# Optimization experiments

Hardware: AMD Instinct MI355X
Metric: run time of the kernel (lower is better)

## Reference

```python
import jax, jax.numpy as jnp
import numpy as np

EMBED_DIM = 1024
NUM_HEADS = 16
HEAD_DIM = EMBED_DIM // NUM_HEADS  # 64
B, H_P, W_P = 4, 48, 48
N = H_P * W_P  # 2304


def setup_inputs() -> dict:
    key = jax.random.key(0)
    ks = jax.random.split(key, 12)
    s = 1.0 / np.sqrt(EMBED_DIM)
    inp = {
        "query": jax.random.normal(ks[0], (B, N, EMBED_DIM), jnp.float32),
        "key": jax.random.normal(ks[1], (B, N, EMBED_DIM), jnp.float32),
        "value": jax.random.normal(ks[2], (B, N, EMBED_DIM), jnp.float32),
        "Wq": jax.random.normal(ks[3], (EMBED_DIM, EMBED_DIM), jnp.float32) * s,
        "bq": jnp.zeros((EMBED_DIM,), jnp.float32),
        "Wk": jax.random.normal(ks[4], (EMBED_DIM, EMBED_DIM), jnp.float32) * s,
        "bk": jnp.zeros((EMBED_DIM,), jnp.float32),
        "Wv": jax.random.normal(ks[5], (EMBED_DIM, EMBED_DIM), jnp.float32) * s,
        "bv": jnp.zeros((EMBED_DIM,), jnp.float32),
        "Wo": jax.random.normal(ks[6], (EMBED_DIM, EMBED_DIM), jnp.float32) * s,
        "bo": jnp.zeros((EMBED_DIM,), jnp.float32),
        "H_patch": H_P,
        "W_patch": W_P,
    }
    return inp


def _rope_2d_cos_sin(h_idx, w_idx, head_dim):
    # 2D RoPE: first half of head_dim encodes the y axis, second half the x axis.
    half = head_dim // 2          # dims per spatial axis (32)
    inv_freq = 1.0 / (10000.0 ** (jnp.arange(0, half, 2, dtype=jnp.float32) / half))  # [half//2]
    fh = h_idx.astype(jnp.float32)[:, None] * inv_freq[None, :]  # [N, half//2]
    fw = w_idx.astype(jnp.float32)[:, None] * inv_freq[None, :]
    emb_h = jnp.concatenate([fh, fh], axis=-1)  # [N, half]
    emb_w = jnp.concatenate([fw, fw], axis=-1)
    emb = jnp.concatenate([emb_h, emb_w], axis=-1)  # [N, head_dim]
    return jnp.cos(emb), jnp.sin(emb)


def _rotate_half_seg(x):
    # rotate_half within a per-axis segment
    h = x.shape[-1] // 2
    return jnp.concatenate([-x[..., h:], x[..., :h]], axis=-1)


def _apply_rotary_2d(x, cos, sin):
    # x: [B, H, N, head_dim]; cos/sin: [N, head_dim]
    half = x.shape[-1] // 2
    c = cos[None, None]
    s = sin[None, None]
    xh, xw = x[..., :half], x[..., half:]
    ch, cw = c[..., :half], c[..., half:]
    sh, sw = s[..., :half], s[..., half:]
    yh = xh * ch + _rotate_half_seg(xh) * sh
    yw = xw * cw + _rotate_half_seg(xw) * sw
    return jnp.concatenate([yh, yw], axis=-1)


def reference(query, key, value, Wq, bq, Wk, bk, Wv, bv, Wo, bo, H_patch, W_patch):
    Bsz, Nn, D = query.shape
    hd = D // NUM_HEADS

    def split_heads(x):
        return x.reshape(Bsz, Nn, NUM_HEADS, hd).transpose(0, 2, 1, 3)  # [B,H,N,hd]

    q = split_heads(query @ Wq.T + bq)
    k = split_heads(key @ Wk.T + bk)
    v = split_heads(value @ Wv.T + bv)

    ys = jnp.arange(H_patch)
    xs = jnp.arange(W_patch)
    yy, xx = jnp.meshgrid(ys, xs, indexing="ij")
    cos, sin = _rope_2d_cos_sin(yy.reshape(-1), xx.reshape(-1), hd)

    q = _apply_rotary_2d(q, cos, sin)
    k = _apply_rotary_2d(k, cos, sin)

    scale = hd ** (-0.5)
    attn = jnp.einsum("bhnd,bhmd->bhnm", q, k) * scale
    attn = jax.nn.softmax(attn, axis=-1)
    out = jnp.einsum("bhnm,bhmd->bhnd", attn, v)
    out = out.transpose(0, 2, 1, 3).reshape(Bsz, Nn, D)
    return out @ Wo.T + bo
```

## Files before the change

kernel.cpp:

```cpp
#include <hip/hip_runtime.h>
#include <cstdint>
#include <cstddef>


typedef __bf16 bf16x8 __attribute__((ext_vector_type(8)));
typedef __bf16 bf16x4 __attribute__((ext_vector_type(4)));
typedef _Float16 f16x4 __attribute__((ext_vector_type(4)));
typedef _Float16 f16x8 __attribute__((ext_vector_type(8)));
typedef float f32x4 __attribute__((ext_vector_type(4)));

constexpr int Bc = 4, Hc = 16, Nc = 2304, Ec = 1024, WPc = 48;
constexpr int BNc = Bc * Nc;

__device__ __forceinline__ f32x4 mfma16(bf16x8 a, bf16x8 b, f32x4 c) {
  return __builtin_amdgcn_mfma_f32_16x16x32_bf16(a, b, c, 0, 0, 0);
}
__device__ __forceinline__ f32x4 mfmah32(f16x8 a, f16x8 b, f32x4 c) {
  return __builtin_amdgcn_mfma_f32_16x16x32_f16(a, b, c, 0, 0, 0);
}

#if __has_builtin(__builtin_amdgcn_exp2f)
#define EXP2F(x) __builtin_amdgcn_exp2f(x)
#else
#define EXP2F(x) exp2f(x)
#endif

#define GPTR(p) ((const __attribute__((address_space(1))) void*)(p))
#define LPTR(p) ((__attribute__((address_space(3))) void*)(p))

__global__ __launch_bounds__(256) void cvt_all(
    const float* __restrict__ s0, const float* __restrict__ s1,
    const float* __restrict__ s2, const float* __restrict__ s3,
    const float* __restrict__ s4, const float* __restrict__ s5,
    const float* __restrict__ s6, __bf16* __restrict__ d) {
  const size_t EE = (size_t)Ec * Ec, BNE = (size_t)BNc * Ec;
  const size_t g = ((size_t)blockIdx.x * 256 + threadIdx.x) * 8;
  const float* s;
  size_t off;
  if (g < 4 * EE) {
    const size_t a = g >> 20;
    off = g & (EE - 1);
    s = (a == 0) ? s0 : (a == 1) ? s1 : (a == 2) ? s2 : s3;
  } else {
    const size_t h = g - 4 * EE;
    const size_t a = h / BNE;
    off = h - a * BNE;
    s = (a == 0) ? s4 : (a == 1) ? s5 : s6;
  }
  float4 f0 = *(const float4*)(s + off);
  float4 f1 = *(const float4*)(s + off + 4);
  bf16x8 v;
  v[0] = (__bf16)f0.x; v[1] = (__bf16)f0.y; v[2] = (__bf16)f0.z; v[3] = (__bf16)f0.w;
  v[4] = (__bf16)f1.x; v[5] = (__bf16)f1.y; v[6] = (__bf16)f1.z; v[7] = (__bf16)f1.w;
  *(bf16x8*)(d + g) = v;
}

#define GEMM_CORE(APTR, WPTR, KDIM)                                             \
  __shared__ __align__(16) __bf16 As[128 * 32];                                 \
  __shared__ __align__(16) __bf16 Bs[128 * 32];                                 \
  const int t = threadIdx.x;                                                    \
  const int lane = t & 63, wave = t >> 6;                                       \
  const int wm = wave & 1, wn = wave >> 1;                                      \
  const int quad = lane >> 4, l15 = lane & 15;                                  \
  const int rowInC = lane >> 2, colC = (lane & 3) * 8;                          \
  const __bf16* Ab = (APTR) + (size_t)(tm * 128) * (KDIM);                      \
  const __bf16* Wb = (WPTR) + (size_t)(tn * 128) * (KDIM);                      \
  f32x4 zero = {0.f, 0.f, 0.f, 0.f};                                            \
  f32x4 acc[4][4];                                                              \
  for (int i = 0; i < 4; ++i)                                                   \
    for (int j = 0; j < 4; ++j) acc[i][j] = zero;                               \
  for (int kk = 0; kk < (KDIM); kk += 32) {                                     \
    _Pragma("unroll") for (int tch = 0; tch < 2; ++tch) {                       \
      const int ch = wave * 2 + tch;                                            \
      const int row = ch * 16 + rowInC;                                         \
      __builtin_amdgcn_global_load_lds(GPTR(Ab + (size_t)row * (KDIM) + kk + colC), \
                                       LPTR(As + ch * 512), 16, 0, 0);          \
      __builtin_amdgcn_global_load_lds(GPTR(Wb + (size_t)row * (KDIM) + kk + colC), \
                                       LPTR(Bs + ch * 512), 16, 0, 0);          \
    }                                                                           \
    __syncthreads();                                                            \
    bf16x8 af[4], bfg[4];                                                       \
    _Pragma("unroll") for (int i = 0; i < 4; ++i)                               \
        af[i] = *(const bf16x8*)(As + (wm * 64 + i * 16 + l15) * 32 + quad * 8);\
    _Pragma("unroll") for (int j = 0; j < 4; ++j)                               \
        bfg[j] = *(const bf16x8*)(Bs + (wn * 64 + j * 16 + l15) * 32 + quad * 8);\
    _Pragma("unroll") for (int i = 0; i < 4; ++i)                               \
      _Pragma("unroll") for (int j = 0; j < 4; ++j)                             \
        acc[i][j] = mfma16(af[i], bfg[j], acc[i][j]);                           \
    __syncthreads();                                                            \
  }                                                                             \
  const int m0 = tm * 128 + wm * 64;                                            \
  const int nb0 = tn * 128 + wn * 64;

__global__ __launch_bounds__(256) void gemm_qk(const __bf16* __restrict__ qkb,
                                               const __bf16* __restrict__ Wqk,
                                               const float* __restrict__ bq,
                                               const float* __restrict__ bk,
                                               __bf16* __restrict__ Qhp,
                                               __bf16* __restrict__ Khp,
                                               float qscale) {
  const int tn = blockIdx.x & 15;
  const int tm = blockIdx.x >> 4;
  const int proj = tn >> 3;
  const __bf16* Asel = qkb + (size_t)proj * BNc * Ec;
  GEMM_CORE(Asel, Wqk, Ec)

  const int h = (nb0 >> 6) & 15;
  const float* bb = proj ? bk : bq;
  float bj[4];
#pragma unroll
  for (int j = 0; j < 4; ++j) bj[j] = bb[(nb0 + j * 16 + l15) & 1023];
  const float f = exp2f(-(float)l15 * 0.8304820237218406f);
  const int lo3 = l15 & 7, hi8 = l15 >> 3;
#pragma unroll
  for (int i = 0; i < 4; ++i) {
#pragma unroll
    for (int r = 0; r < 4; ++r) {
      const int m = m0 + i * 16 + quad * 4 + r;
      const int b = m / Nc;
      const int ntok = m - b * Nc;
      const int ph = ntok / WPc, pw = ntok - (ntok / WPc) * WPc;
      float sh, ch, sw, cw;
      __sincosf((float)ph * f, &sh, &ch);
      __sincosf((float)pw * f, &sw, &cw);
      const float x0 = acc[i][0][r] + bj[0];
      const float x1 = acc[i][1][r] + bj[1];
      const float x2 = acc[i][2][r] + bj[2];
      const float x3 = acc[i][3][r] + bj[3];
      const float y0 = x0 * ch - x1 * sh;
      const float y1 = x1 * ch + x0 * sh;
      const float y2 = x2 * cw - x3 * sw;
      const float y3 = x3 * cw + x2 * sw;
      if (proj == 0) {
        __bf16* Op = Qhp + ((size_t)(b * Hc + h) * Nc + ntok) * 64;
        Op[l15]      = (__bf16)(y0 * qscale);
        Op[l15 + 16] = (__bf16)(y1 * qscale);
        Op[l15 + 32] = (__bf16)(y2 * qscale);
        Op[l15 + 48] = (__bf16)(y3 * qscale);
      } else {
        const int t64 = ntok & 63;
        const int p64 = (t64 & 35) | ((t64 & 4) << 2) | ((t64 & 24) >> 1);
        __bf16* Kp = Khp + ((size_t)(b * Hc + h) * 36 + (ntok >> 6)) * 4096 +
                     (size_t)((((p64 >> 4) * 2) * 64 + hi8 * 16 + (p64 & 15)) * 8 + lo3);
        Kp[0]   = (__bf16)y0;
        Kp[256] = (__bf16)y1;
        Kp[512] = (__bf16)y2;
        Kp[768] = (__bf16)y3;
      }
    }
  }
}

__global__ __launch_bounds__(256) void gemm_v(const __bf16* __restrict__ A,
                                              const __bf16* __restrict__ Wv,
                                              const float* __restrict__ bv,
                                              _Float16* __restrict__ Vt) {
  const int tn = blockIdx.x & 7;
  const int tm = blockIdx.x >> 3;
  GEMM_CORE(A, Wv, Ec)

  const int h = nb0 >> 6;
#pragma unroll
  for (int i = 0; i < 4; ++i) {
    const int m = m0 + i * 16 + quad * 4;
    const int b = m / Nc;
    const int ntok = m - b * Nc;
    const int t64 = ntok & 63;
    const int c2 = t64 >> 5, qf = (t64 >> 3) & 3, jf0 = t64 & 7;
    const size_t vbase = ((size_t)(b * Hc + h) * 36 + (ntok >> 6)) * 4096;
#pragma unroll
    for (int j = 0; j < 4; ++j) {
      const float bi = bv[nb0 + j * 16 + l15];
      f16x4 v;
#pragma unroll
      for (int r = 0; r < 4; ++r) v[r] = (_Float16)(acc[i][j][r] + bi);
      *(f16x4*)(Vt + vbase +
                (size_t)(((c2 * 4 + j) * 64 + qf * 16 + l15) * 8 + jf0)) = v;
    }
  }
}

__global__ __launch_bounds__(256) void gemm_out(const __bf16* __restrict__ A,
                                                const __bf16* __restrict__ Wo,
                                                const float* __restrict__ bo,
                                                float* __restrict__ C) {
  const int tn = blockIdx.x & 7;
  const int tm = blockIdx.x >> 3;
  GEMM_CORE(A, Wo, Ec)

#pragma unroll
  for (int j = 0; j < 4; ++j) {
    const int n = nb0 + j * 16 + l15;
    const float bi = bo[n];
#pragma unroll
    for (int i = 0; i < 4; ++i) {
      const int m = m0 + i * 16 + quad * 4;
#pragma unroll
      for (int r = 0; r < 4; ++r) C[(size_t)(m + r) * Ec + n] = acc[i][j][r] + bi;
    }
  }
}

constexpr int TQ = 128, TK = 64, NT = Nc / TK;

__global__ __launch_bounds__(256) void attn(const __bf16* __restrict__ Qh,
                                            const __bf16* __restrict__ Kf,
                                            const _Float16* __restrict__ Vf,
                                            __bf16* __restrict__ Om) {
  const int bh = blockIdx.x;
  const int t = threadIdx.x, wave = t >> 6, lane = t & 63;
  const int quad = lane >> 4, l15 = lane & 15;
  const int qbase = blockIdx.y * TQ + wave * 32;

  bf16x8 bq[2][2];
#pragma unroll
  for (int s = 0; s < 2; ++s)
#pragma unroll
    for (int ks = 0; ks < 2; ++ks)
      bq[s][ks] = *(const bf16x8*)(Qh + ((size_t)bh * Nc + qbase + s * 16 + l15) * 64 +
                                   ks * 32 + quad * 8);

  const __bf16* Kb = Kf + (size_t)bh * (NT * 4096) + (size_t)lane * 8;
  const _Float16* Vb = Vf + (size_t)bh * (NT * 4096) + (size_t)lane * 8;

  const f32x4 zero = {0.f, 0.f, 0.f, 0.f};
  f32x4 oacc[2][4] = {{zero, zero, zero, zero}, {zero, zero, zero, zero}};
  f32x4 osum[2] = {zero, zero};
  const f16x8 fones8 = {(_Float16)1.f, (_Float16)1.f, (_Float16)1.f, (_Float16)1.f,
                        (_Float16)1.f, (_Float16)1.f, (_Float16)1.f, (_Float16)1.f};

#define LOADKV(KF, VF, KT)                                                      \
  {                                                                             \
    _Pragma("unroll") for (int f = 0; f < 8; ++f)                               \
      KF[f] = *(const bf16x8*)(Kb + (size_t)(KT) * 4096 + f * 512);             \
    _Pragma("unroll") for (int f = 0; f < 8; ++f)                               \
      VF[f] = *(const f16x8*)(Vb + (size_t)(KT) * 4096 + f * 512);              \
  }

#define COMPUTE(KF, VF)                                                         \
  {                                                                             \
    f32x4 sacc[2][4] = {{zero, zero, zero, zero}, {zero, zero, zero, zero}};    \
    __builtin_amdgcn_s_setprio(1);                                              \
    _Pragma("unroll") for (int ks = 0; ks < 2; ++ks)                            \
      _Pragma("unroll") for (int ct = 0; ct < 4; ++ct) {                        \
        sacc[0][ct] = mfma16(KF[ct * 2 + ks], bq[0][ks], sacc[0][ct]);          \
        sacc[1][ct] = mfma16(KF[ct * 2 + ks], bq[1][ks], sacc[1][ct]);          \
      }                                                                         \
    __builtin_amdgcn_s_setprio(0);                                              \
    f16x8 pf[2][2];                                                             \
    _Pragma("unroll") for (int s = 0; s < 2; ++s)                               \
      _Pragma("unroll") for (int c2 = 0; c2 < 2; ++c2) {                        \
        _Pragma("unroll") for (int r = 0; r < 4; ++r) {                         \
          pf[s][c2][r]     = (_Float16)EXP2F(sacc[s][2 * c2][r]);               \
          pf[s][c2][4 + r] = (_Float16)EXP2F(sacc[s][2 * c2 + 1][r]);           \
        }                                                                       \
      }                                                                         \
    __builtin_amdgcn_s_setprio(1);                                              \
    _Pragma("unroll") for (int c2 = 0; c2 < 2; ++c2) {                          \
      _Pragma("unroll") for (int dt = 0; dt < 4; ++dt) {                        \
        oacc[0][dt] = mfmah32(VF[c2 * 4 + dt], pf[0][c2], oacc[0][dt]);         \
        oacc[1][dt] = mfmah32(VF[c2 * 4 + dt], pf[1][c2], oacc[1][dt]);         \
      }                                                                         \
      osum[0] = mfmah32(fones8, pf[0][c2], osum[0]);                            \
      osum[1] = mfmah32(fones8, pf[1][c2], osum[1]);                            \
    }                                                                           \
    __builtin_amdgcn_s_setprio(0);                                              \
  }

  bf16x8 kfA[8], kfB[8];
  f16x8 vfA[8], vfB[8];
  LOADKV(kfA, vfA, 0)

#pragma unroll 1
  for (int kt = 0; kt < NT; kt += 2) {
    LOADKV(kfB, vfB, kt + 1)
    COMPUTE(kfA, vfA)
    if (kt + 2 < NT) LOADKV(kfA, vfA, kt + 2)
    COMPUTE(kfB, vfB)
  }

  const int b = bh >> 4, h = bh & 15;
#pragma unroll
  for (int s = 0; s < 2; ++s) {
    const float rinv = 1.0f / osum[s][0];
    __bf16* Op = Om + ((size_t)b * Nc + qbase + s * 16 + l15) * Ec + h * 64 + quad * 4;
#pragma unroll
    for (int dt = 0; dt < 4; ++dt) {
      bf16x4 o;
#pragma unroll
      for (int r = 0; r < 4; ++r) o[r] = (__bf16)(oacc[s][dt][r] * rinv);
      *(bf16x4*)(Op + dt * 16) = o;
    }
  }
#undef LOADKV
#undef COMPUTE
}

extern "C" void kernel_launch(void* const* d_in, const int* in_sizes, int n_in,
                              void* d_out, int out_size, void* d_ws, size_t ws_size,
                              hipStream_t stream) {
  const float* q  = (const float*)d_in[0];
  const float* k  = (const float*)d_in[1];
  const float* v  = (const float*)d_in[2];
  const float* Wq = (const float*)d_in[3];
  const float* bq = (const float*)d_in[4];
  const float* Wk = (const float*)d_in[5];
  const float* bk = (const float*)d_in[6];
  const float* Wv = (const float*)d_in[7];
  const float* bv = (const float*)d_in[8];
  const float* Wo = (const float*)d_in[9];
  const float* bo = (const float*)d_in[10];
  float* out = (float*)d_out;

  const size_t EE = (size_t)Ec * Ec;
  const size_t BNE = (size_t)BNc * Ec;

  char* w = (char*)d_ws;
  __bf16* Wqkb = (__bf16*)w; w += 2 * EE * 2;
  __bf16* Wvb  = (__bf16*)w; w += EE * 2;
  __bf16* Wob  = (__bf16*)w; w += EE * 2;
  __bf16* qb   = (__bf16*)w; w += BNE * 2;
  __bf16* kb   = (__bf16*)w; w += BNE * 2;
  __bf16* vb   = (__bf16*)w; w += BNE * 2;
  __bf16* Qhp  = (__bf16*)w; w += BNE * 2;
  __bf16* Khp  = (__bf16*)w; w += BNE * 2;
  _Float16* Vtp = (_Float16*)kb;
  __bf16* Omp = qb;

  const dim3 blk(256);
  const dim3 gCvt((4 * EE + 3 * BNE) / 8 / 256);
  const dim3 gQK(16 * (BNc / 128));
  const dim3 gG(8 * (BNc / 128));
  const dim3 gAttn(Bc * Hc, Nc / TQ);

  cvt_all<<<gCvt, blk, 0, stream>>>(Wq, Wk, Wv, Wo, q, k, v, Wqkb);

  const float qscale = 0.125f * 1.44269504088896340736f;

  gemm_qk<<<gQK, blk, 0, stream>>>(qb, Wqkb, bq, bk, Qhp, Khp, qscale);
  gemm_v<<<gG, blk, 0, stream>>>(vb, Wvb, bv, Vtp);
  attn<<<gAttn, blk, 0, stream>>>(Qhp, Khp, Vtp, Omp);
  gemm_out<<<gG, blk, 0, stream>>>(Omp, Wob, bo, out);
}
```

Baseline: 423.2 us.

## Fuse Q/K/V projection GEMMs into one launch and interleave attention exp with PV MFMAs

```diff
diff --git a/kernel.cpp b/kernel.cpp
--- a/kernel.cpp
+++ b/kernel.cpp
@@ -92,20 +92,44 @@
   const int m0 = tm * 128 + wm * 64;                                            \
   const int nb0 = tn * 128 + wn * 64;
 
-__global__ __launch_bounds__(256) void gemm_qk(const __bf16* __restrict__ qkb,
-                                               const __bf16* __restrict__ Wqk,
-                                               const float* __restrict__ bq,
-                                               const float* __restrict__ bk,
-                                               __bf16* __restrict__ Qhp,
-                                               __bf16* __restrict__ Khp,
-                                               float qscale) {
-  const int tn = blockIdx.x & 15;
-  const int tm = blockIdx.x >> 4;
+__global__ __launch_bounds__(256) void gemm_qkv(const __bf16* __restrict__ qkvb,
+                                                const __bf16* __restrict__ Wqkv,
+                                                const float* __restrict__ bq,
+                                                const float* __restrict__ bk,
+                                                const float* __restrict__ bv,
+                                                __bf16* __restrict__ Qhp,
+                                                __bf16* __restrict__ Khp,
+                                                _Float16* __restrict__ Vtp,
+                                                float qscale) {
+  const int tn = blockIdx.x % 24;
+  const int tm = blockIdx.x / 24;
   const int proj = tn >> 3;
-  const __bf16* Asel = qkb + (size_t)proj * BNc * Ec;
-  GEMM_CORE(Asel, Wqk, Ec)
+  const __bf16* Asel = qkvb + (size_t)proj * BNc * Ec;
+  GEMM_CORE(Asel, Wqkv, Ec)
 
   const int h = (nb0 >> 6) & 15;
+  if (proj == 2) {
+#pragma unroll
+    for (int i = 0; i < 4; ++i) {
+      const int m = m0 + i * 16 + quad * 4;
+      const int b = m / Nc;
+      const int ntok = m - b * Nc;
+      const int t64 = ntok & 63;
+      const int c2 = t64 >> 5, qf = (t64 >> 3) & 3, jf0 = t64 & 7;
+      const size_t vbase = ((size_t)(b * Hc + h) * 36 + (ntok >> 6)) * 4096;
+#pragma unroll
+      for (int j = 0; j < 4; ++j) {
+        const float bi = bv[(nb0 + j * 16 + l15) & 1023];
+        f16x4 v;
+#pragma unroll
+        for (int r = 0; r < 4; ++r) v[r] = (_Float16)(acc[i][j][r] + bi);
+        *(f16x4*)(Vtp + vbase +
+                  (size_t)(((c2 * 4 + j) * 64 + qf * 16 + l15) * 8 + jf0)) = v;
+      }
+    }
+    return;
+  }
+
   const float* bb = proj ? bk : bq;
   float bj[4];
 #pragma unroll
@@ -151,35 +175,6 @@
   }
 }
 
-__global__ __launch_bounds__(256) void gemm_v(const __bf16* __restrict__ A,
-                                              const __bf16* __restrict__ Wv,
-                                              const float* __restrict__ bv,
-                                              _Float16* __restrict__ Vt) {
-  const int tn = blockIdx.x & 7;
-  const int tm = blockIdx.x >> 3;
-  GEMM_CORE(A, Wv, Ec)
-
-  const int h = nb0 >> 6;
-#pragma unroll
-  for (int i = 0; i < 4; ++i) {
-    const int m = m0 + i * 16 + quad * 4;
-    const int b = m / Nc;
-    const int ntok = m - b * Nc;
-    const int t64 = ntok & 63;
-    const int c2 = t64 >> 5, qf = (t64 >> 3) & 3, jf0 = t64 & 7;
-    const size_t vbase = ((size_t)(b * Hc + h) * 36 + (ntok >> 6)) * 4096;
-#pragma unroll
-    for (int j = 0; j < 4; ++j) {
-      const float bi = bv[nb0 + j * 16 + l15];
-      f16x4 v;
-#pragma unroll
-      for (int r = 0; r < 4; ++r) v[r] = (_Float16)(acc[i][j][r] + bi);
-      *(f16x4*)(Vt + vbase +
-                (size_t)(((c2 * 4 + j) * 64 + qf * 16 + l15) * 8 + jf0)) = v;
-    }
-  }
-}
-
 __global__ __launch_bounds__(256) void gemm_out(const __bf16* __restrict__ A,
                                                 const __bf16* __restrict__ Wo,
                                                 const float* __restrict__ bo,
@@ -240,31 +235,25 @@
 #define COMPUTE(KF, VF)                                                         \
   {                                                                             \
     f32x4 sacc[2][4] = {{zero, zero, zero, zero}, {zero, zero, zero, zero}};    \
-    __builtin_amdgcn_s_setprio(1);                                              \
     _Pragma("unroll") for (int ks = 0; ks < 2; ++ks)                            \
       _Pragma("unroll") for (int ct = 0; ct < 4; ++ct) {                        \
         sacc[0][ct] = mfma16(KF[ct * 2 + ks], bq[0][ks], sacc[0][ct]);          \
         sacc[1][ct] = mfma16(KF[ct * 2 + ks], bq[1][ks], sacc[1][ct]);          \
       }                                                                         \
-    __builtin_amdgcn_s_setprio(0);                                              \
-    f16x8 pf[2][2];                                                             \
-    _Pragma("unroll") for (int s = 0; s < 2; ++s)                               \
-      _Pragma("unroll") for (int c2 = 0; c2 < 2; ++c2) {                        \
+    _Pragma("unroll") for (int c2 = 0; c2 < 2; ++c2) {                          \
+      f16x8 pf[2];                                                              \
+      _Pragma("unroll") for (int s = 0; s < 2; ++s)                             \
         _Pragma("unroll") for (int r = 0; r < 4; ++r) {                         \
-          pf[s][c2][r]     = (_Float16)EXP2F(sacc[s][2 * c2][r]);               \
-          pf[s][c2][4 + r] = (_Float16)EXP2F(sacc[s][2 * c2 + 1][r]);           \
+          pf[s][r]     = (_Float16)EXP2F(sacc[s][2 * c2][r]);                   \
+          pf[s][4 + r] = (_Float16)EXP2F(sacc[s][2 * c2 + 1][r]);               \
         }                                                                       \
+      _Pragma("unroll") for (int dt = 0; dt < 4; ++dt) {                        \
+        oacc[0][dt] = mfmah32(VF[c2 * 4 + dt], pf[0], oacc[0][dt]);             \
+        oacc[1][dt] = mfmah32(VF[c2 * 4 + dt], pf[1], oacc[1][dt]);             \
       }                                                                         \
-    __builtin_amdgcn_s_setprio(1);                                              \
-    _Pragma("unroll") for (int c2 = 0; c2 < 2; ++c2) {                          \
-      _Pragma("unroll") for (int dt = 0; dt < 4; ++dt) {                        \
-        oacc[0][dt] = mfmah32(VF[c2 * 4 + dt], pf[0][c2], oacc[0][dt]);         \
-        oacc[1][dt] = mfmah32(VF[c2 * 4 + dt], pf[1][c2], oacc[1][dt]);         \
-      }                                                                         \
-      osum[0] = mfmah32(fones8, pf[0][c2], osum[0]);                            \
-      osum[1] = mfmah32(fones8, pf[1][c2], osum[1]);                            \
+      osum[0] = mfmah32(fones8, pf[0], osum[0]);                                \
+      osum[1] = mfmah32(fones8, pf[1], osum[1]);                                \
     }                                                                           \
-    __builtin_amdgcn_s_setprio(0);                                              \
   }
 
   bf16x8 kfA[8], kfB[8];
@@ -324,12 +313,14 @@
   __bf16* vb   = (__bf16*)w; w += BNE * 2;
   __bf16* Qhp  = (__bf16*)w; w += BNE * 2;
   __bf16* Khp  = (__bf16*)w; w += BNE * 2;
-  _Float16* Vtp = (_Float16*)kb;
+  __bf16* Vfp  = (__bf16*)w; w += BNE * 2;
+  _Float16* Vtp = (_Float16*)Vfp;
   __bf16* Omp = qb;
+  (void)Wvb;
 
   const dim3 blk(256);
   const dim3 gCvt((4 * EE + 3 * BNE) / 8 / 256);
-  const dim3 gQK(16 * (BNc / 128));
+  const dim3 gQKV(24 * (BNc / 128));
   const dim3 gG(8 * (BNc / 128));
   const dim3 gAttn(Bc * Hc, Nc / TQ);
 
@@ -337,8 +328,7 @@
 
   const float qscale = 0.125f * 1.44269504088896340736f;
 
-  gemm_qk<<<gQK, blk, 0, stream>>>(qb, Wqkb, bq, bk, Qhp, Khp, qscale);
-  gemm_v<<<gG, blk, 0, stream>>>(vb, Wvb, bv, Vtp);
+  gemm_qkv<<<gQKV, blk, 0, stream>>>(qb, Wqkb, bq, bk, bv, Qhp, Khp, Vtp, qscale);
   attn<<<gAttn, blk, 0, stream>>>(Qhp, Khp, Vtp, Omp);
   gemm_out<<<gG, blk, 0, stream>>>(Omp, Wob, bo, out);
 }
```

After: 502.8 us. +18.8%, slower.
